# Kernel tuning notes

Measured on AMD Instinct MI355X. Metric: run time of the kernel, lower is better.

The kernel has to match this reference:

```python
import jax, jax.numpy as jnp
import numpy as np

B, N, D, H = 16, 1024, 384, 6
DH = D // H  # 64 per-head dim


def _layernorm(x, w, b, eps=1e-5):
    mu = jnp.mean(x, axis=-1, keepdims=True)
    var = jnp.var(x, axis=-1, keepdims=True)
    return (x - mu) * jax.lax.rsqrt(var + eps) * w + b


def setup_inputs() -> dict:
    key = jax.random.key(0)
    ks = jax.random.split(key, 10)
    std = 0.02
    return {
        "X": jax.random.normal(ks[0], (B, N, D), dtype=jnp.float32),
        "Wq": jax.random.normal(ks[1], (H, DH, D), dtype=jnp.float32) * std,
        "Wk": jax.random.normal(ks[2], (H, DH, D), dtype=jnp.float32) * std,
        "Wv": jax.random.normal(ks[3], (H, DH, D), dtype=jnp.float32) * std,
        "Wo": jax.random.normal(ks[4], (D, D), dtype=jnp.float32) * std,
        "bo": jnp.zeros((D,), dtype=jnp.float32),
        "ln1_w": jnp.ones((D,), dtype=jnp.float32),
        "ln1_b": jnp.zeros((D,), dtype=jnp.float32),
        "ln2_w": jnp.ones((D,), dtype=jnp.float32),
        "ln2_b": jnp.zeros((D,), dtype=jnp.float32),
        "W1": jax.random.normal(ks[5], (2 * D, D), dtype=jnp.float32) * std,
        "b1": jnp.zeros((2 * D,), dtype=jnp.float32),
        "W2": jax.random.normal(ks[6], (D, 2 * D), dtype=jnp.float32) * std,
        "b2": jnp.zeros((D,), dtype=jnp.float32),
    }


def reference(X, Wq, Wk, Wv, Wo, bo, ln1_w, ln1_b, ln2_w, ln2_b, W1, b1, W2, b2):
    scale = 1.0 / jnp.sqrt(jnp.float32(DH))
    # pre-LN then multi-head attention (heads vectorized, math identical to per-head loop)
    t = _layernorm(X, ln1_w, ln1_b)                       # [B,N,D]
    q = jnp.einsum('bnd,hkd->bhnk', t, Wq)                # [B,H,N,DH]
    k = jnp.einsum('bnd,hkd->bhnk', t, Wk)
    v = jnp.einsum('bnd,hkd->bhnk', t, Wv)
    scores = jnp.einsum('bhnk,bhmk->bhnm', q, k) * scale  # [B,H,N,N]
    p = jax.nn.softmax(scores, axis=-1)
    o = jnp.einsum('bhnm,bhmk->bhnk', p, v)               # [B,H,N,DH]
    o = jnp.transpose(o, (0, 2, 1, 3)).reshape(B, N, D)   # concat heads
    attn = o @ Wo.T + bo
    # residual + post-LN (dropout/drop_path are identity in eval)
    X2 = _layernorm(X + attn, ln2_w, ln2_b)
    # MLP: Linear -> exact GELU -> Linear
    h = jax.nn.gelu(X2 @ W1.T + b1, approximate=False)
    mlp = h @ W2.T + b2
    return X2 + mlp
```

## Files before the change

### kernel.cpp

```cpp
#include <hip/hip_runtime.h>
#include <math.h>

typedef float  f32x4  __attribute__((ext_vector_type(4)));
typedef __bf16 bf16x8 __attribute__((ext_vector_type(8)));
typedef __bf16 bf16x4 __attribute__((ext_vector_type(4)));

__device__ __forceinline__ void gload16(const void* g, void* l) {
  __builtin_amdgcn_global_load_lds((__attribute__((address_space(1))) const void*)g,
                                   (__attribute__((address_space(3))) void*)l, 16, 0, 0);
}

__device__ __forceinline__ f32x4 mfma16(bf16x8 a, bf16x8 b, f32x4 c) {
  return __builtin_amdgcn_mfma_f32_16x16x32_bf16(a, b, c, 0, 0, 0);
}

__device__ __forceinline__ f32x4 mfma8(long a, long b, f32x4 c) {
  return __builtin_amdgcn_mfma_f32_16x16x32_fp8_fp8(a, b, c, 0, 0, 0);
}

__device__ __forceinline__ unsigned char f2fp8(float x) {
  return (unsigned char)__builtin_amdgcn_cvt_pk_fp8_f32(x, x, 0, false);
}

__device__ __forceinline__ float fast_gelu(float x) {
  const float xs = x * 0.70710678118654752f;
  const float ax = fabsf(xs);
  const float t  = __builtin_amdgcn_rcpf(1.f + 0.3275911f * ax);
  const float poly = ((((1.061405429f*t - 1.453152027f)*t + 1.421413741f)*t
                       - 0.284496736f)*t + 0.254829592f)*t;
  const float e = __builtin_amdgcn_exp2f(-1.4426950408889634f * ax * ax);
  float erfv = 1.f - poly * e;
  erfv = (xs < 0.f) ? -erfv : erfv;
  return 0.5f * x * (1.f + erfv);
}

__global__ __launch_bounds__(256) void prep_kernel(
    const float* __restrict__ X, const float* __restrict__ ln1w, const float* __restrict__ ln1b,
    unsigned char* __restrict__ t8,
    const float* __restrict__ Wq, const float* __restrict__ Wk, const float* __restrict__ Wv,
    const float* __restrict__ Wo, const float* __restrict__ W1, const float* __restrict__ W2,
    unsigned char* __restrict__ wqkv8, unsigned char* __restrict__ wo8,
    unsigned char* __restrict__ w18, unsigned char* __restrict__ w28)
{
  if (blockIdx.x >= 4096) {
    const int idx = ((blockIdx.x - 4096) * 256 + threadIdx.x) * 4;
    const float* src; unsigned char* dst; int off;
    if      (idx < 147456) { src = Wq; dst = wqkv8;          off = idx; }
    else if (idx < 294912) { src = Wk; dst = wqkv8 + 147456; off = idx - 147456; }
    else if (idx < 442368) { src = Wv; dst = wqkv8 + 294912; off = idx - 294912; }
    else if (idx < 589824) { src = Wo; dst = wo8;            off = idx - 442368; }
    else if (idx < 884736) { src = W1; dst = w18;            off = idx - 589824; }
    else                   { src = W2; dst = w28;            off = idx - 884736; }
    f32x4 v = *(const f32x4*)(src + off);
    int p = __builtin_amdgcn_cvt_pk_fp8_f32(v.x, v.y, 0, false);
    p     = __builtin_amdgcn_cvt_pk_fp8_f32(v.z, v.w, p, true);
    *(int*)(dst + off) = p;
    return;
  }
  const int row  = blockIdx.x * 4 + (threadIdx.x >> 6);
  const int lane = threadIdx.x & 63;
  const float* x = X + (size_t)row * 384;
  float v[6]; float s = 0.f;
#pragma unroll
  for (int j = 0; j < 6; ++j) { v[j] = x[lane + 64*j]; s += v[j]; }
#pragma unroll
  for (int off = 32; off > 0; off >>= 1) s += __shfl_xor(s, off);
  const float mu = s * (1.f/384.f);
  float s2 = 0.f;
#pragma unroll
  for (int j = 0; j < 6; ++j) { float d = v[j] - mu; s2 += d*d; }
#pragma unroll
  for (int off = 32; off > 0; off >>= 1) s2 += __shfl_xor(s2, off);
  const float inv = rsqrtf(s2 * (1.f/384.f) + 1e-5f);
#pragma unroll
  for (int j = 0; j < 6; ++j) {
    const int cidx = lane + 64*j;
    t8[(size_t)row*384 + cidx] = f2fp8((v[j]-mu)*inv*ln1w[cidx] + ln1b[cidx]);
  }
}

__global__ __launch_bounds__(256) void ln_kernel(
    const float* __restrict__ in, const float* __restrict__ w, const float* __restrict__ b,
    unsigned char* __restrict__ outc, float* __restrict__ outf)
{
  const int row  = blockIdx.x * 4 + (threadIdx.x >> 6);
  const int lane = threadIdx.x & 63;
  const float* x = in + (size_t)row * 384;
  float v[6]; float s = 0.f;
#pragma unroll
  for (int j = 0; j < 6; ++j) { v[j] = x[lane + 64*j]; s += v[j]; }
#pragma unroll
  for (int off = 32; off > 0; off >>= 1) s += __shfl_xor(s, off);
  const float mu = s * (1.f/384.f);
  float s2 = 0.f;
#pragma unroll
  for (int j = 0; j < 6; ++j) { float d = v[j] - mu; s2 += d*d; }
#pragma unroll
  for (int off = 32; off > 0; off >>= 1) s2 += __shfl_xor(s2, off);
  const float inv = rsqrtf(s2 * (1.f/384.f) + 1e-5f);
#pragma unroll
  for (int j = 0; j < 6; ++j) {
    const int cidx = lane + 64*j;
    const float y = (v[j]-mu)*inv*w[cidx] + b[cidx];
    outc[(size_t)row*384 + cidx] = f2fp8(y);
    outf[(size_t)row*384 + cidx] = y;
  }
}

template<int EPI>
__global__ __launch_bounds__(256, 3) void gemm_f8(
    const unsigned char* __restrict__ A, const unsigned char* __restrict__ Bw,
    int N, int K,
    const float* __restrict__ bias, const float* __restrict__ resid,
    float* __restrict__ outf, unsigned char* __restrict__ outc,
    __bf16* __restrict__ q_out, __bf16* __restrict__ k_out, __bf16* __restrict__ vt_out)
{
  __shared__ __attribute__((aligned(16))) unsigned char As[2][8192];
  __shared__ __attribute__((aligned(16))) unsigned char Bs[2][8192];
  const int tid  = threadIdx.x;
  const int lane = tid & 63;
  const int w    = tid >> 6;
  const int wm   = w >> 1, wn = w & 1;
  const int m0   = blockIdx.x * 128, n0 = blockIdx.y * 128;

  f32x4 acc[4][4] = {};

  const int srow = lane & 15, skq = (lane >> 4) << 4;
  const unsigned char* gptr[4];
  unsigned char*       lptr[4];
#pragma unroll
  for (int r = 0; r < 4; ++r) {
    const int id = r * 4 + w;
    if (id < 8) { gptr[r] = A  + (size_t)(m0 + id*16 + srow) * K + skq; lptr[r] = &As[0][id * 1024]; }
    else        { const int j = id - 8;
                  gptr[r] = Bw + (size_t)(n0 + j*16 + srow) * K + skq; lptr[r] = &Bs[0][j * 1024]; }
  }

  auto stage = [&](int kk, int b) {
#pragma unroll
    for (int r = 0; r < 4; ++r)
      gload16(gptr[r] + kk * 64, lptr[r] + b * 8192);
  };
  const int lo = lane & 15, quad = lane >> 4;
  const int foff = (quad >> 1) * 256 + lo * 16 + (quad & 1) * 8;
  auto compute = [&](int b) {
#pragma unroll
    for (int s = 0; s < 2; ++s) {
      long af[4], bfr[4];
#pragma unroll
      for (int i = 0; i < 4; ++i)
        af[i]  = *(const long*)&As[b][(wm*4 + i) * 1024 + s * 512 + foff];
#pragma unroll
      for (int j = 0; j < 4; ++j)
        bfr[j] = *(const long*)&Bs[b][(wn*4 + j) * 1024 + s * 512 + foff];
#pragma unroll
      for (int i = 0; i < 4; ++i)
#pragma unroll
        for (int j = 0; j < 4; ++j)
          acc[i][j] = mfma8(af[i], bfr[j], acc[i][j]);
    }
  };

  const int NIT = K >> 6;
  stage(0, 0);
  __syncthreads();
  for (int k = 0; k < NIT; ++k) {
    const int b = k & 1;
    if (k + 1 < NIT) stage(k + 1, b ^ 1);
    compute(b);
    __syncthreads();
  }

#pragma unroll
  for (int rt = 0; rt < 4; ++rt) {
#pragma unroll
    for (int ct = 0; ct < 4; ++ct) {
      const int gr0 = m0 + (wm*4 + rt)*16 + quad*4;
      const int gc  = n0 + (wn*4 + ct)*16 + lo;
      f32x4 a = acc[rt][ct];
      if constexpr (EPI == 0) {
        const int bb = gr0 >> 10, nn = gr0 & 1023;
        if (gc >= 768) {
          const int jj = gc - 768, hh = jj >> 6, dh = jj & 63;
          bf16x4 pk = {(__bf16)a[0], (__bf16)a[1], (__bf16)a[2], (__bf16)a[3]};
          *(bf16x4*)&vt_out[((size_t)((bb*6 + hh)*64 + dh) << 10) + nn] = pk;
        } else {
          const bool isq = (gc < 384);
          const int jj = isq ? gc : (gc - 384);
          __bf16* dst = isq ? q_out : k_out;
          const float sc = isq ? 0.18033688011112042f : 1.0f;
          const int hh = jj >> 6, dh = jj & 63;
#pragma unroll
          for (int i = 0; i < 4; ++i)
            dst[((size_t)(((bb*6 + hh) << 10) | (nn + i)) << 6) + dh] = (__bf16)(a[i] * sc);
        }
      } else {
#pragma unroll
        for (int i = 0; i < 4; ++i) {
          const int gr = gr0 + i;
          float val = a[i];
          if constexpr (EPI == 1) {
            const size_t idx = (size_t)gr * N + gc;
            outf[idx] = val + bias[gc] + resid[idx];
          } else if constexpr (EPI == 2) {
            outc[(size_t)gr * N + gc] = f2fp8(fast_gelu(val + bias[gc]));
          } else {
            const size_t idx = (size_t)gr * N + gc;
            outf[idx] = outf[idx] + val + bias[gc];
          }
        }
      }
    }
  }
}

__global__ __launch_bounds__(256, 3) void attn_kernel(
    const __bf16* __restrict__ qp, const __bf16* __restrict__ kp,
    const __bf16* __restrict__ vtp, unsigned char* __restrict__ omat8)
{
  __shared__ __attribute__((aligned(16))) __bf16 Ks[2][4096];
  __shared__ __attribute__((aligned(16))) __bf16 Vs[2][4096];
  __shared__ __attribute__((aligned(16))) __bf16 Ps[4][2][1088];
  const int tid = threadIdx.x, lane = tid & 63, w = tid >> 6;
  const int bh = blockIdx.x;
  const int q0 = blockIdx.y * 128 + w * 32;
  const int quad = lane >> 4, lo = lane & 15;

  bf16x8 qa[2][2];
#pragma unroll
  for (int t = 0; t < 2; ++t) {
    const __bf16* qb = qp + ((size_t)bh * 1024 + q0 + t*16 + lo) * 64 + (quad << 3);
    qa[t][0] = *(const bf16x8*)qb;
    qa[t][1] = *(const bf16x8*)(qb + 32);
  }

  f32x4 oacc[2][4] = {};
  float l_r[2] = {0.f, 0.f};

  auto stage = [&](int c, int bb) {
#pragma unroll
    for (int s = 0; s < 2; ++s) {
      const int ck = s * 256 + tid;
      const int l = ck & 63, g = ck >> 6;
      const int ct = g >> 1, ks = g & 1;
      const __bf16* gk = kp + ((size_t)bh*1024 + c*64 + ct*16 + (l & 15)) * 64
                            + ks*32 + ((l >> 4) << 3);
      gload16(gk, &Ks[bb][(ck & ~63) * 8]);
      const __bf16* gv = vtp + (((size_t)(bh*64 + ct*16 + (l & 15))) << 10)
                             + c*64 + ks*32 + ((l >> 4) << 3);
      gload16(gv, &Vs[bb][(ck & ~63) * 8]);
    }
  };

  stage(0, 0);
  __syncthreads();

  for (int c = 0; c < 16; ++c) {
    const int bb = c & 1;
    if (c + 1 < 16) stage(c + 1, bb ^ 1);

    f32x4 st[2][4];
#pragma unroll
    for (int ct = 0; ct < 4; ++ct) {
      bf16x8 kb0 = *(const bf16x8*)&Ks[bb][((ct*2 + 0)*64 + lane) * 8];
      bf16x8 kb1 = *(const bf16x8*)&Ks[bb][((ct*2 + 1)*64 + lane) * 8];
#pragma unroll
      for (int t = 0; t < 2; ++t) {
        f32x4 s0 = {};
        s0 = mfma16(kb0, qa[t][0], s0);
        s0 = mfma16(kb1, qa[t][1], s0);
        st[t][ct] = s0;
      }
    }
#pragma unroll
    for (int t = 0; t < 2; ++t)
#pragma unroll
      for (int ct = 0; ct < 4; ++ct) {
        const float p0 = __builtin_amdgcn_exp2f(st[t][ct][0]);
        const float p1 = __builtin_amdgcn_exp2f(st[t][ct][1]);
        const float p2 = __builtin_amdgcn_exp2f(st[t][ct][2]);
        const float p3 = __builtin_amdgcn_exp2f(st[t][ct][3]);
        l_r[t] += (p0 + p1) + (p2 + p3);
        bf16x4 pk = {(__bf16)p0, (__bf16)p1, (__bf16)p2, (__bf16)p3};
        *(bf16x4*)&Ps[w][t][lo*68 + ct*16 + quad*4] = pk;
      }
    bf16x8 pa[2][2];
#pragma unroll
    for (int t = 0; t < 2; ++t)
#pragma unroll
      for (int ks = 0; ks < 2; ++ks)
        pa[t][ks] = *(const bf16x8*)&Ps[w][t][lo*68 + ks*32 + (quad << 3)];
#pragma unroll
    for (int dt = 0; dt < 4; ++dt)
#pragma unroll
      for (int ks = 0; ks < 2; ++ks) {
        bf16x8 vb = *(const bf16x8*)&Vs[bb][((dt*2 + ks)*64 + lane) * 8];
#pragma unroll
        for (int t = 0; t < 2; ++t)
          oacc[t][dt] = mfma16(pa[t][ks], vb, oacc[t][dt]);
      }
    __syncthreads();
  }

  const int b = bh / 6, h = bh - (bh / 6) * 6;
#pragma unroll
  for (int t = 0; t < 2; ++t) {
    float ls = l_r[t];
    ls += __shfl_xor(ls, 16);
    ls += __shfl_xor(ls, 32);
#pragma unroll
    for (int i = 0; i < 4; ++i) {
      const float linv = 1.f / __shfl(ls, quad*4 + i);
      const int n = q0 + t*16 + quad*4 + i;
#pragma unroll
      for (int dt = 0; dt < 4; ++dt)
        omat8[((size_t)((b << 10) | n)) * 384 + (h << 6) + dt*16 + lo] =
            f2fp8(oacc[t][dt][i] * linv);
    }
  }
}

extern "C" void kernel_launch(void* const* d_in, const int* in_sizes, int n_in,
                              void* d_out, int out_size, void* d_ws, size_t ws_size,
                              hipStream_t stream)
{
  const float* X    = (const float*)d_in[0];
  const float* Wq   = (const float*)d_in[1];
  const float* Wk   = (const float*)d_in[2];
  const float* Wv   = (const float*)d_in[3];
  const float* Wo   = (const float*)d_in[4];
  const float* bo   = (const float*)d_in[5];
  const float* ln1w = (const float*)d_in[6];
  const float* ln1b = (const float*)d_in[7];
  const float* ln2w = (const float*)d_in[8];
  const float* ln2b = (const float*)d_in[9];
  const float* W1   = (const float*)d_in[10];
  const float* b1   = (const float*)d_in[11];
  const float* W2   = (const float*)d_in[12];
  const float* b2   = (const float*)d_in[13];

  char* ws = (char*)d_ws;
  unsigned char* t8   = (unsigned char*)(ws + 0);
  unsigned char* x2_f8 = (unsigned char*)(ws + 6291456);
  __bf16* q_bf  = (__bf16*)(ws + 12582912);
  __bf16* k_bf  = (__bf16*)(ws + 25165824);
  unsigned char* omat8 = (unsigned char*)(ws + 37748736);
  __bf16* vt_bf = (__bf16*)(ws + 50331648);
  float*  s1    = (float*) (ws + 62914560);
  unsigned char* h8 = (unsigned char*)(ws + 62914560);
  unsigned char* wqkv8 = (unsigned char*)(ws + 88080384);
  unsigned char* wo8 = (unsigned char*)(ws + 88522752);
  unsigned char* w18 = (unsigned char*)(ws + 88670208);
  unsigned char* w28 = (unsigned char*)(ws + 88965120);
  float*  out   = (float*)d_out;

  prep_kernel<<<5248, 256, 0, stream>>>(X, ln1w, ln1b, t8,
      Wq, Wk, Wv, Wo, W1, W2, wqkv8, wo8, w18, w28);
  gemm_f8<0><<<dim3(128,9), 256, 0, stream>>>(t8, wqkv8, 1152, 384,
      nullptr, nullptr, nullptr, nullptr, q_bf, k_bf, vt_bf);
  attn_kernel<<<dim3(96,8), 256, 0, stream>>>(q_bf, k_bf, vt_bf, omat8);
  gemm_f8<1><<<dim3(128,3), 256, 0, stream>>>(omat8, wo8, 384, 384,
      bo, X, s1, nullptr, nullptr, nullptr, nullptr);
  ln_kernel<<<4096, 256, 0, stream>>>(s1, ln2w, ln2b, x2_f8, out);
  gemm_f8<2><<<dim3(128,6), 256, 0, stream>>>(x2_f8, w18, 768, 384,
      b1, nullptr, nullptr, h8, nullptr, nullptr, nullptr);
  gemm_f8<3><<<dim3(128,3), 256, 0, stream>>>(h8, w28, 384, 768,
      b2, nullptr, out, nullptr, nullptr, nullptr, nullptr);
}
```

Measured before the change: 240.4 us.

## Prefetch K two chunks ahead and split barrier around the softmax stage

The attention kernel now stages K and V separately. K is triple-buffered and loaded two chunks ahead, while V stays double-buffered and is loaded one chunk ahead. The single __syncthreads per iteration becomes an explicit vmcnt wait plus barrier placed before the PV MFMAs, plus a trailing barrier, so the exp/softmax work overlaps outstanding V loads. The per-wave P scratch drops to a single slot reused by both row tiles, which keeps total LDS roughly unchanged. Correctness now depends on hand-tuned vmcnt counts matching the issued loads.

```diff
diff --git a/kernel.cpp b/kernel.cpp
--- a/kernel.cpp
+++ b/kernel.cpp
@@ -218,9 +218,9 @@
     const __bf16* __restrict__ qp, const __bf16* __restrict__ kp,
     const __bf16* __restrict__ vtp, unsigned char* __restrict__ omat8)
 {
-  __shared__ __attribute__((aligned(16))) __bf16 Ks[2][4096];
+  __shared__ __attribute__((aligned(16))) __bf16 Ks[3][4096];
   __shared__ __attribute__((aligned(16))) __bf16 Vs[2][4096];
-  __shared__ __attribute__((aligned(16))) __bf16 Ps[4][2][1088];
+  __shared__ __attribute__((aligned(16))) __bf16 Ps[4][1088];
   const int tid = threadIdx.x, lane = tid & 63, w = tid >> 6;
   const int bh = blockIdx.x;
   const int q0 = blockIdx.y * 128 + w * 32;
@@ -237,7 +237,7 @@
   f32x4 oacc[2][4] = {};
   float l_r[2] = {0.f, 0.f};
 
-  auto stage = [&](int c, int bb) {
+  auto stageK = [&](int c, int kb) {
 #pragma unroll
     for (int s = 0; s < 2; ++s) {
       const int ck = s * 256 + tid;
@@ -245,25 +245,36 @@
       const int ct = g >> 1, ks = g & 1;
       const __bf16* gk = kp + ((size_t)bh*1024 + c*64 + ct*16 + (l & 15)) * 64
                             + ks*32 + ((l >> 4) << 3);
-      gload16(gk, &Ks[bb][(ck & ~63) * 8]);
+      gload16(gk, &Ks[kb][(ck & ~63) * 8]);
+    }
+  };
+  auto stageV = [&](int c, int vb) {
+#pragma unroll
+    for (int s = 0; s < 2; ++s) {
+      const int ck = s * 256 + tid;
+      const int l = ck & 63, g = ck >> 6;
+      const int ct = g >> 1, ks = g & 1;
       const __bf16* gv = vtp + (((size_t)(bh*64 + ct*16 + (l & 15))) << 10)
                              + c*64 + ks*32 + ((l >> 4) << 3);
-      gload16(gv, &Vs[bb][(ck & ~63) * 8]);
+      gload16(gv, &Vs[vb][(ck & ~63) * 8]);
     }
   };
 
-  stage(0, 0);
-  __syncthreads();
+  stageK(0, 0); stageK(1, 1); stageV(0, 0);
+  asm volatile("s_waitcnt vmcnt(0)" ::: "memory");
+  __builtin_amdgcn_s_barrier();
 
   for (int c = 0; c < 16; ++c) {
-    const int bb = c & 1;
-    if (c + 1 < 16) stage(c + 1, bb ^ 1);
+    const int kb = c % 3;
+    const int vb = c & 1;
+    if (c + 2 < 16) stageK(c + 2, (c + 2) % 3);
+    if (c + 1 < 16) stageV(c + 1, (c + 1) & 1);
 
     f32x4 st[2][4];
 #pragma unroll
     for (int ct = 0; ct < 4; ++ct) {
-      bf16x8 kb0 = *(const bf16x8*)&Ks[bb][((ct*2 + 0)*64 + lane) * 8];
-      bf16x8 kb1 = *(const bf16x8*)&Ks[bb][((ct*2 + 1)*64 + lane) * 8];
+      bf16x8 kb0 = *(const bf16x8*)&Ks[kb][((ct*2 + 0)*64 + lane) * 8];
+      bf16x8 kb1 = *(const bf16x8*)&Ks[kb][((ct*2 + 1)*64 + lane) * 8];
 #pragma unroll
       for (int t = 0; t < 2; ++t) {
         f32x4 s0 = {};
@@ -272,8 +283,9 @@
         st[t][ct] = s0;
       }
     }
-#pragma unroll
-    for (int t = 0; t < 2; ++t)
+    bf16x8 pa[2][2];
+#pragma unroll
+    for (int t = 0; t < 2; ++t) {
 #pragma unroll
       for (int ct = 0; ct < 4; ++ct) {
         const float p0 = __builtin_amdgcn_exp2f(st[t][ct][0]);
@@ -282,24 +294,30 @@
         const float p3 = __builtin_amdgcn_exp2f(st[t][ct][3]);
         l_r[t] += (p0 + p1) + (p2 + p3);
         bf16x4 pk = {(__bf16)p0, (__bf16)p1, (__bf16)p2, (__bf16)p3};
-        *(bf16x4*)&Ps[w][t][lo*68 + ct*16 + quad*4] = pk;
+        *(bf16x4*)&Ps[w][lo*68 + ct*16 + quad*4] = pk;
       }
-    bf16x8 pa[2][2];
-#pragma unroll
-    for (int t = 0; t < 2; ++t)
 #pragma unroll
       for (int ks = 0; ks < 2; ++ks)
-        pa[t][ks] = *(const bf16x8*)&Ps[w][t][lo*68 + ks*32 + (quad << 3)];
+        pa[t][ks] = *(const bf16x8*)&Ps[w][lo*68 + ks*32 + (quad << 3)];
+    }
+
+    if (c <= 13)      asm volatile("s_waitcnt vmcnt(4)" ::: "memory");
+    else if (c == 14) asm volatile("s_waitcnt vmcnt(2)" ::: "memory");
+    else              asm volatile("s_waitcnt vmcnt(0)" ::: "memory");
+    __builtin_amdgcn_sched_barrier(0);
+    __builtin_amdgcn_s_barrier();
+
 #pragma unroll
     for (int dt = 0; dt < 4; ++dt)
 #pragma unroll
       for (int ks = 0; ks < 2; ++ks) {
-        bf16x8 vb = *(const bf16x8*)&Vs[bb][((dt*2 + ks)*64 + lane) * 8];
+        bf16x8 vbv = *(const bf16x8*)&Vs[vb][((dt*2 + ks)*64 + lane) * 8];
 #pragma unroll
         for (int t = 0; t < 2; ++t)
-          oacc[t][dt] = mfma16(pa[t][ks], vb, oacc[t][dt]);
+          oacc[t][dt] = mfma16(pa[t][ks], vbv, oacc[t][dt]);
       }
-    __syncthreads();
+
+    __builtin_amdgcn_s_barrier();
   }
 
   const int b = bh / 6, h = bh - (bh / 6) * 6;
```

Measured after the change: 238.4 us. No clear change (-0.8%).

## Triple-buffer GEMM and attention loads; keep softmax P in registers for PV MFMA

Applied to the files above, without the earlier changes.

Both the fp8 GEMM and the attention kernel move from double to triple buffering of LDS tiles. They prefetch two stages ahead and use explicit vmcnt waits with raw barriers instead of __syncthreads. The attention kernel also drops the per-wave LDS round trip for the probability matrix: the exp'd scores are reused directly as A operands of the 16x16x16 bf16 MFMA, which matches the score accumulator layout, with V fragments read in a matching layout. This costs more LDS (3 buffers), which may reduce occupancy, and uses half-K MFMAs, doubling the PV MFMA instruction count.

```diff
diff --git a/kernel.cpp b/kernel.cpp
--- a/kernel.cpp
+++ b/kernel.cpp
@@ -4,6 +4,7 @@
 typedef float  f32x4  __attribute__((ext_vector_type(4)));
 typedef __bf16 bf16x8 __attribute__((ext_vector_type(8)));
 typedef __bf16 bf16x4 __attribute__((ext_vector_type(4)));
+typedef short  s16x4  __attribute__((ext_vector_type(4)));
 
 __device__ __forceinline__ void gload16(const void* g, void* l) {
   __builtin_amdgcn_global_load_lds((__attribute__((address_space(1))) const void*)g,
@@ -12,6 +13,15 @@
 
 __device__ __forceinline__ f32x4 mfma16(bf16x8 a, bf16x8 b, f32x4 c) {
   return __builtin_amdgcn_mfma_f32_16x16x32_bf16(a, b, c, 0, 0, 0);
+}
+
+__device__ __forceinline__ f32x4 pv_mfma(s16x4 a, s16x4 b, f32x4 c) {
+#if __has_builtin(__builtin_amdgcn_mfma_f32_16x16x16bf16_1k)
+  return __builtin_amdgcn_mfma_f32_16x16x16bf16_1k(a, b, c, 0, 0, 0);
+#else
+  asm("s_nop 1\n\tv_mfma_f32_16x16x16_bf16 %0, %1, %2, %0" : "+v"(c) : "v"(a), "v"(b));
+  return c;
+#endif
 }
 
 __device__ __forceinline__ f32x4 mfma8(long a, long b, f32x4 c) {
@@ -115,8 +125,8 @@
     float* __restrict__ outf, unsigned char* __restrict__ outc,
     __bf16* __restrict__ q_out, __bf16* __restrict__ k_out, __bf16* __restrict__ vt_out)
 {
-  __shared__ __attribute__((aligned(16))) unsigned char As[2][8192];
-  __shared__ __attribute__((aligned(16))) unsigned char Bs[2][8192];
+  __shared__ __attribute__((aligned(16))) unsigned char As[3][8192];
+  __shared__ __attribute__((aligned(16))) unsigned char Bs[3][8192];
   const int tid  = threadIdx.x;
   const int lane = tid & 63;
   const int w    = tid >> 6;
@@ -162,13 +172,22 @@
   };
 
   const int NIT = K >> 6;
-  stage(0, 0);
-  __syncthreads();
+  stage(0, 0); stage(1, 1);
+  asm volatile("s_waitcnt vmcnt(4)" ::: "memory");
+  __builtin_amdgcn_sched_barrier(0);
+  __builtin_amdgcn_s_barrier();
+  int rb = 0;
   for (int k = 0; k < NIT; ++k) {
-    const int b = k & 1;
-    if (k + 1 < NIT) stage(k + 1, b ^ 1);
-    compute(b);
-    __syncthreads();
+    const int sb = (rb == 0) ? 2 : rb - 1;
+    if (k + 2 < NIT) stage(k + 2, sb);
+    compute(rb);
+    if (k + 2 < NIT)      asm volatile("s_waitcnt vmcnt(4)" ::: "memory");
+    else if (k + 1 < NIT) asm volatile("s_waitcnt vmcnt(0)" ::: "memory");
+    if (k + 1 < NIT) {
+      __builtin_amdgcn_sched_barrier(0);
+      __builtin_amdgcn_s_barrier();
+    }
+    rb = (rb == 2) ? 0 : rb + 1;
   }
 
 #pragma unroll
@@ -218,9 +237,8 @@
     const __bf16* __restrict__ qp, const __bf16* __restrict__ kp,
     const __bf16* __restrict__ vtp, unsigned char* __restrict__ omat8)
 {
-  __shared__ __attribute__((aligned(16))) __bf16 Ks[2][4096];
-  __shared__ __attribute__((aligned(16))) __bf16 Vs[2][4096];
-  __shared__ __attribute__((aligned(16))) __bf16 Ps[4][2][1088];
+  __shared__ __attribute__((aligned(16))) __bf16 Ks[3][4096];
+  __shared__ __attribute__((aligned(16))) __bf16 Vs[3][4096];
   const int tid = threadIdx.x, lane = tid & 63, w = tid >> 6;
   const int bh = blockIdx.x;
   const int q0 = blockIdx.y * 128 + w * 32;
@@ -237,7 +255,7 @@
   f32x4 oacc[2][4] = {};
   float l_r[2] = {0.f, 0.f};
 
-  auto stage = [&](int c, int bb) {
+  auto stage = [&](int c, int b) {
 #pragma unroll
     for (int s = 0; s < 2; ++s) {
       const int ck = s * 256 + tid;
@@ -245,25 +263,30 @@
       const int ct = g >> 1, ks = g & 1;
       const __bf16* gk = kp + ((size_t)bh*1024 + c*64 + ct*16 + (l & 15)) * 64
                             + ks*32 + ((l >> 4) << 3);
-      gload16(gk, &Ks[bb][(ck & ~63) * 8]);
+      gload16(gk, &Ks[b][(ck & ~63) * 8]);
       const __bf16* gv = vtp + (((size_t)(bh*64 + ct*16 + (l & 15))) << 10)
                              + c*64 + ks*32 + ((l >> 4) << 3);
-      gload16(gv, &Vs[bb][(ck & ~63) * 8]);
+      gload16(gv, &Vs[b][(ck & ~63) * 8]);
     }
   };
 
-  stage(0, 0);
-  __syncthreads();
-
+  const int vbase = lo*8 + (quad >> 1)*128 + (quad & 1)*4;
+
+  stage(0, 0); stage(1, 1);
+  asm volatile("s_waitcnt vmcnt(4)" ::: "memory");
+  __builtin_amdgcn_sched_barrier(0);
+  __builtin_amdgcn_s_barrier();
+
+  int rb = 0;
   for (int c = 0; c < 16; ++c) {
-    const int bb = c & 1;
-    if (c + 1 < 16) stage(c + 1, bb ^ 1);
+    const int sb = (rb == 0) ? 2 : rb - 1;
+    if (c + 2 < 16) stage(c + 2, sb);
 
     f32x4 st[2][4];
 #pragma unroll
     for (int ct = 0; ct < 4; ++ct) {
-      bf16x8 kb0 = *(const bf16x8*)&Ks[bb][((ct*2 + 0)*64 + lane) * 8];
-      bf16x8 kb1 = *(const bf16x8*)&Ks[bb][((ct*2 + 1)*64 + lane) * 8];
+      bf16x8 kb0 = *(const bf16x8*)&Ks[rb][((ct*2 + 0)*64 + lane) * 8];
+      bf16x8 kb1 = *(const bf16x8*)&Ks[rb][((ct*2 + 1)*64 + lane) * 8];
 #pragma unroll
       for (int t = 0; t < 2; ++t) {
         f32x4 s0 = {};
@@ -272,6 +295,7 @@
         st[t][ct] = s0;
       }
     }
+    s16x4 pa4[2][4];
 #pragma unroll
     for (int t = 0; t < 2; ++t)
 #pragma unroll
@@ -282,24 +306,26 @@
         const float p3 = __builtin_amdgcn_exp2f(st[t][ct][3]);
         l_r[t] += (p0 + p1) + (p2 + p3);
         bf16x4 pk = {(__bf16)p0, (__bf16)p1, (__bf16)p2, (__bf16)p3};
-        *(bf16x4*)&Ps[w][t][lo*68 + ct*16 + quad*4] = pk;
+        pa4[t][ct] = __builtin_bit_cast(s16x4, pk);
       }
-    bf16x8 pa[2][2];
-#pragma unroll
-    for (int t = 0; t < 2; ++t)
-#pragma unroll
-      for (int ks = 0; ks < 2; ++ks)
-        pa[t][ks] = *(const bf16x8*)&Ps[w][t][lo*68 + ks*32 + (quad << 3)];
-#pragma unroll
-    for (int dt = 0; dt < 4; ++dt)
-#pragma unroll
-      for (int ks = 0; ks < 2; ++ks) {
-        bf16x8 vb = *(const bf16x8*)&Vs[bb][((dt*2 + ks)*64 + lane) * 8];
+
+#pragma unroll
+    for (int ct = 0; ct < 4; ++ct)
+#pragma unroll
+      for (int dt = 0; dt < 4; ++dt) {
+        s16x4 vf = *(const s16x4*)&Vs[rb][dt*1024 + ct*256 + vbase];
 #pragma unroll
         for (int t = 0; t < 2; ++t)
-          oacc[t][dt] = mfma16(pa[t][ks], vb, oacc[t][dt]);
+          oacc[t][dt] = pv_mfma(pa4[t][ct], vf, oacc[t][dt]);
       }
-    __syncthreads();
+
+    if (c + 2 < 16)       asm volatile("s_waitcnt vmcnt(4)" ::: "memory");
+    else if (c + 1 < 16)  asm volatile("s_waitcnt vmcnt(0)" ::: "memory");
+    if (c + 1 < 16) {
+      __builtin_amdgcn_sched_barrier(0);
+      __builtin_amdgcn_s_barrier();
+    }
+    rb = (rb == 2) ? 0 : rb + 1;
   }
 
   const int b = bh / 6, h = bh - (bh / 6) * 6;
```

Measured after the change: 246.5 us. +2.5%, slower.
